# Kernel tuning notes

Measured on AMD Instinct MI355X. Metric: run time of the kernel, lower is better.

The kernel has to match this reference:

```python
import jax, jax.numpy as jnp
import numpy as np

HEADS, DIM_HEAD, LANDMARKS, PINV_ITERS = 8, 64, 256, 6


def moore_penrose_pinv(x, iters=PINV_ITERS):
    abs_x = jnp.abs(x)
    col = abs_x.sum(-1)
    row = abs_x.sum(-2)
    z = jnp.swapaxes(x, -1, -2) / (jnp.max(col) * jnp.max(row))
    I = jnp.eye(x.shape[-1], dtype=x.dtype)
    for _ in range(iters):
        xz = x @ z
        z = 0.25 * z @ (13 * I - xz @ (15 * I - xz @ (7 * I - xz)))
    return z


def nystrom_attention(x, w_qkv, w_out, b_out, res_conv_w):
    b, n, dim = x.shape
    m = LANDMARKS
    pad = (m - n % m) % m
    x = jnp.pad(x, ((0, 0), (pad, 0), (0, 0)))  # pad at front like F.pad(x,(0,0,pad,0))
    npad = n + pad
    qkv = x @ w_qkv  # (b, npad, 3*heads*dim_head)
    q, k, v = jnp.split(qkv, 3, axis=-1)
    sh = lambda t: t.reshape(b, npad, HEADS, DIM_HEAD).transpose(0, 2, 1, 3)
    q, k, v = sh(q), sh(k), sh(v)  # (b,h,npad,dh)
    q = q * (DIM_HEAD ** -0.5)
    l = npad // m
    q_l = q.reshape(b, HEADS, m, l, DIM_HEAD).mean(axis=3)  # landmarks (b,h,m,dh)
    k_l = k.reshape(b, HEADS, m, l, DIM_HEAD).mean(axis=3)
    attn1 = jax.nn.softmax(jnp.einsum('bhid,bhjd->bhij', q, k_l), -1)   # (b,h,npad,m)
    attn2 = jax.nn.softmax(jnp.einsum('bhid,bhjd->bhij', q_l, k_l), -1)  # (b,h,m,m)
    attn3 = jax.nn.softmax(jnp.einsum('bhid,bhjd->bhij', q_l, k), -1)   # (b,h,m,npad)
    out = attn1 @ (moore_penrose_pinv(attn2) @ (attn3 @ v))  # (b,h,npad,dh)
    # depthwise residual conv over sequence dim (Conv2d(heads,heads,(33,1),groups=heads,bias=False))
    res = jax.lax.conv_general_dilated(v, res_conv_w, (1, 1), ((16, 16), (0, 0)),
                                       dimension_numbers=('NCHW', 'OIHW', 'NCHW'),
                                       feature_group_count=HEADS)
    out = out + res
    out = out.transpose(0, 2, 1, 3).reshape(b, npad, HEADS * DIM_HEAD)
    out = out @ w_out + b_out
    return out[:, -n:]


def camil_forward(bag, adj_row, adj_col, adj_val, w_qkv, w_out, b_out, res_conv_w,
                  wq, wk, wv_w, wv_b, v_att, u_att, w_att, fc_kernel, fc_bias):
    N = bag.shape[1]
    # encoder
    xg = nystrom_attention(bag, w_qkv, w_out, b_out, res_conv_w)[0]  # (N,D)
    enc = xg + bag  # (1,N,D)
    q = enc @ wq  # (1,N,256)
    k = enc @ wk
    attn = jnp.einsum('bnd,bmd->bnm', q, k)[0] / jnp.sqrt(jnp.float32(256.0))  # (N,N)
    # sparse adjacency-masked neighbor aggregation
    edge_scores = adj_val * attn[adj_row, adj_col]
    A_raw = jax.ops.segment_sum(edge_scores, adj_row, num_segments=N)  # (N,)
    alpha = jax.nn.softmax(A_raw)
    value = bag @ wv_w + wv_b  # (1,N,D)
    xl = alpha[:, None] * value  # (1,N,D)
    wei2 = jax.nn.sigmoid(-xl) ** 2
    xo = xl * 2 * wei2 + 2 * enc * (1 - wei2)  # (1,N,D)
    # gated MIL attention (softmax over dim 0 of size 1, as in original)
    inst = jnp.tanh(xo @ v_att) * jax.nn.sigmoid(xo @ u_att)
    scores = inst @ w_att  # (1,N,1)
    k_alpha = jax.nn.softmax(scores, axis=0)
    attn_output = k_alpha * xo
    pooled = attn_output[0].sum(axis=0, keepdims=True)  # (1,D)
    out = pooled @ fc_kernel + fc_bias  # (1,1)
    return out, A_raw, k_alpha


def setup_inputs() -> dict:
    key = jax.random.key(0)
    ks = jax.random.split(key, 16)
    N, D, E = 10000, 512, 90000
    s = 0.02
    return {
        'bag': jax.random.normal(ks[0], (1, N, D), jnp.float32),
        'adj_row': jax.random.randint(ks[1], (E,), 0, N),
        'adj_col': jax.random.randint(ks[2], (E,), 0, N),
        'adj_val': jax.random.uniform(ks[3], (E,), jnp.float32),
        'w_qkv': jax.random.normal(ks[4], (D, 3 * HEADS * DIM_HEAD), jnp.float32) * s,
        'w_out': jax.random.normal(ks[5], (HEADS * DIM_HEAD, D), jnp.float32) * s,
        'b_out': jnp.zeros((D,), jnp.float32),
        'res_conv_w': jax.random.normal(ks[6], (HEADS, 1, 33, 1), jnp.float32) * s,
        'wq': jax.random.normal(ks[7], (D, 256), jnp.float32) * s,
        'wk': jax.random.normal(ks[8], (D, 256), jnp.float32) * s,
        'wv_w': jax.random.normal(ks[9], (D, D), jnp.float32) * s,
        'wv_b': jnp.zeros((D,), jnp.float32),
        'v_att': jax.random.normal(ks[10], (D, 128), jnp.float32) * s,
        'u_att': jax.random.normal(ks[11], (D, 128), jnp.float32) * s,
        'w_att': jax.random.normal(ks[12], (128, 1), jnp.float32) * s,
        'fc_kernel': jax.random.normal(ks[13], (D, 1), jnp.float32) * s,
        'fc_bias': jnp.zeros((1,), jnp.float32),
    }


def reference(bag, adj_row, adj_col, adj_val, w_qkv, w_out, b_out, res_conv_w,
              wq, wk, wv_w, wv_b, v_att, u_att, w_att, fc_kernel, fc_bias):
    return camil_forward(bag, adj_row, adj_col, adj_val, w_qkv, w_out, b_out, res_conv_w,
                         wq, wk, wv_w, wv_b, v_att, u_att, w_att, fc_kernel, fc_bias)
```

## Files before the change

### kernel.cpp

```cpp
#include <hip/hip_runtime.h>
#include <hip/hip_bf16.h>
#include <math.h>

#define NSEQ   10000
#define NPAD   10240
#define PADR   240
#define HEADS  8
#define DH     64
#define LM     256
#define LFAC   40
#define DMODEL 512
#define DQK    256
#define OUTSZ  20001
#define NSPLIT 16
#define KCH    128

typedef __attribute__((ext_vector_type(8))) short bf16x8;
typedef __attribute__((ext_vector_type(4))) float f32x4;
#define MFMA16(a,b,c) __builtin_amdgcn_mfma_f32_16x16x32_bf16(a,b,c,0,0,0)

typedef __attribute__((address_space(1))) const unsigned char gconst_t;
typedef __attribute__((address_space(3))) unsigned char lds_t;
#define GLD16(gp, lp) __builtin_amdgcn_global_load_lds((gconst_t*)(gp), (lds_t*)(lp), 16, 0, 0)

__device__ __forceinline__ float b2f(ushort u) {
    return __uint_as_float(((unsigned)u) << 16);
}
__device__ __forceinline__ ushort f2b(float f) {
    unsigned u = __float_as_uint(f);
    unsigned r = (u + 0x7FFFu + ((u >> 16) & 1u)) >> 16;
    return (ushort)r;
}
__device__ __forceinline__ int swz8(int bid, int nwg) {
    int q = nwg >> 3, r = nwg & 7;
    int x = bid & 7, idx = bid >> 3;
    int start = (x < r) ? x * (q + 1) : r * (q + 1) + (x - r) * q;
    return start + idx;
}
__device__ __forceinline__ f32x4 tr4(f32x4 v, int p) {
    f32x4 u, w;
    float s, r;
    s = (p & 1) ? v[0] : v[1]; r = __shfl_xor(s, 1);
    u[0] = (p & 1) ? r : v[0]; u[1] = (p & 1) ? v[1] : r;
    s = (p & 1) ? v[2] : v[3]; r = __shfl_xor(s, 1);
    u[2] = (p & 1) ? r : v[2]; u[3] = (p & 1) ? v[3] : r;
    s = (p & 2) ? u[0] : u[2]; r = __shfl_xor(s, 2);
    w[0] = (p & 2) ? r : u[0]; w[2] = (p & 2) ? u[2] : r;
    s = (p & 2) ? u[1] : u[3]; r = __shfl_xor(s, 2);
    w[1] = (p & 2) ? r : u[1]; w[3] = (p & 2) ? u[3] : r;
    return w;
}

__global__ __launch_bounds__(256)
void cvt_k(const float* __restrict__ in, ushort* __restrict__ out, int n4,
           float* __restrict__ outbuf, const float* __restrict__ fcb,
           unsigned int* __restrict__ mx)
{
    int i = blockIdx.x * 256 + threadIdx.x;
    if (i < n4) {
        float4 v = ((const float4*)in)[i];
        ushort4 u; u.x = f2b(v.x); u.y = f2b(v.y); u.z = f2b(v.z); u.w = f2b(v.w);
        ((ushort4*)out)[i] = u;
    }
    if (i == 0) { outbuf[0] = fcb[0]; mx[0] = 0u; mx[1] = 0u; }
    if (i >= 1 && i <= NSEQ) outbuf[i] = 0.f;
    if (i >= NSEQ + 1 && i < OUTSZ) outbuf[i] = 1.0f;
}

__global__ __launch_bounds__(256)
void wtrans_k(const float* __restrict__ w_qkv, const float* __restrict__ w_out,
              const float* __restrict__ wq, const float* __restrict__ wk,
              const float* __restrict__ wv_w,
              ushort* __restrict__ wqkvT, ushort* __restrict__ woutT,
              ushort* __restrict__ wqkT)
{
    __shared__ float tile[32][33];
    int g0 = blockIdx.x * 32, r0 = blockIdx.y * 32;
    const float* in; ushort* outp; int C; int lc0;
    if (g0 < 1536)      { in = w_qkv; outp = wqkvT;                      C = 1536; lc0 = g0; }
    else if (g0 < 2048) { in = w_out; outp = woutT;                      C = 512;  lc0 = g0 - 1536; }
    else if (g0 < 2304) { in = wq;    outp = wqkT;                       C = 256;  lc0 = g0 - 2048; }
    else if (g0 < 2560) { in = wk;    outp = wqkT + 256*512;             C = 256;  lc0 = g0 - 2304; }
    else                { in = wv_w;  outp = wqkvT + (size_t)1536*512;   C = 512;  lc0 = g0 - 2560; }
    int tx = threadIdx.x & 31, ty = threadIdx.x >> 5;
    for (int i = ty; i < 32; i += 8) tile[i][tx] = in[(size_t)(r0 + i) * C + lc0 + tx];
    __syncthreads();
    for (int i = ty; i < 32; i += 8) outp[(size_t)(lc0 + i) * 512 + r0 + tx] = f2b(tile[tx][i]);
}

template<int MODE, int TN>
__global__ __launch_bounds__(256)
void mgemm(const ushort* __restrict__ A, const ushort* __restrict__ Bt,
           int Mlog, int N, int K, int padr, int nbx,
           void* __restrict__ P0, void* __restrict__ P1, void* __restrict__ P2,
           void* __restrict__ P3, void* __restrict__ P4,
           const float* __restrict__ bias, const ushort* __restrict__ extra)
{
    constexpr int NF = TN / 32;
    constexpr int BSB = TN * 64;
    __shared__ __align__(16) char As[2 * 8192];
    __shared__ __align__(16) char Bs[2 * BSB];
    const int tid = threadIdx.x;
    const int l = tid & 63, w = tid >> 6;
    const int wm = w >> 1, wn = w & 1;
    const int wk_ = swz8(blockIdx.x, gridDim.x);
    const int row0 = (wk_ / nbx) * 128, col0 = (wk_ % nbx) * TN;
    const int lr = l & 15, lg = l >> 4;
    const bool slow = (MODE == 0) && (row0 < padr);
    const int NT = K >> 5;
    f32x4 acc[4][NF];
    #pragma unroll
    for (int i = 0; i < 4; ++i)
        #pragma unroll
        for (int j = 0; j < NF; ++j) acc[i][j] = (f32x4){0.f, 0.f, 0.f, 0.f};

    auto stage = [&](int bf, int t) {
        int k0 = t << 5;
        if (!slow) {
            #pragma unroll
            for (int c = 0; c < 2; ++c) {
                int q = w * 2 + c;
                int row = q * 16 + (l >> 2);
                GLD16(A + (size_t)(row0 + row - padr) * K + k0 + (l & 3) * 8,
                      As + bf * 8192 + q * 1024);
            }
            if (TN == 128) {
                #pragma unroll
                for (int c = 0; c < 2; ++c) {
                    int q = w * 2 + c;
                    int row = q * 16 + (l >> 2);
                    GLD16(Bt + (size_t)(col0 + row) * K + k0 + (l & 3) * 8,
                          Bs + bf * BSB + q * 1024);
                }
            } else {
                int row = w * 16 + (l >> 2);
                GLD16(Bt + (size_t)(col0 + row) * K + k0 + (l & 3) * 8,
                      Bs + bf * BSB + w * 1024);
            }
        } else {
            #pragma unroll
            for (int c = 0; c < 2; ++c) {
                int gidx = c * 256 + tid;
                int row = gidx >> 2, gr = gidx & 3;
                int phys = row0 + row - padr;
                uint4 v = {0, 0, 0, 0};
                if (phys >= 0 && phys < Mlog - padr)
                    v = *(const uint4*)(A + (size_t)phys * K + k0 + gr * 8);
                *(uint4*)(As + bf * 8192 + gidx * 16) = v;
            }
            if (TN == 128) {
                #pragma unroll
                for (int c = 0; c < 2; ++c) {
                    int gidx = c * 256 + tid;
                    int row = gidx >> 2, gr = gidx & 3;
                    *(uint4*)(Bs + bf * BSB + gidx * 16) =
                        *(const uint4*)(Bt + (size_t)(col0 + row) * K + k0 + gr * 8);
                }
            } else {
                int row = tid >> 2, gr = tid & 3;
                *(uint4*)(Bs + bf * BSB + tid * 16) =
                    *(const uint4*)(Bt + (size_t)(col0 + row) * K + k0 + gr * 8);
            }
        }
    };

    int cur = 0;
    stage(0, 0);
    __syncthreads();
    for (int t = 0; t < NT; ++t) {
        if (t + 1 < NT) stage(cur ^ 1, t + 1);
        const char* Ab = As + cur * 8192;
        const char* Bb = Bs + cur * BSB;
        bf16x8 af[4];
        #pragma unroll
        for (int mf = 0; mf < 4; ++mf)
            af[mf] = *(const bf16x8*)(Ab + (wm * 64 + mf * 16 + lr) * 64 + lg * 16);
        #pragma unroll
        for (int nf = 0; nf < NF; ++nf) {
            bf16x8 bfr = *(const bf16x8*)(Bb + (wn * (TN / 2) + nf * 16 + lr) * 64 + lg * 16);
            #pragma unroll
            for (int mf = 0; mf < 4; ++mf)
                acc[mf][nf] = MFMA16(af[mf], bfr, acc[mf][nf]);
        }
        __syncthreads();
        cur ^= 1;
    }

    const int p = lr & 3;
    #pragma unroll
    for (int mf = 0; mf < 4; ++mf)
    #pragma unroll
    for (int nf = 0; nf < NF; ++nf) {
        int cb   = col0 + wn * (TN / 2) + nf * 16 + (lr & 12);
        int rowT = row0 + wm * 64 + mf * 16 + lg * 4 + p;
        if (MODE == 0) {
            int c = col0 + wn * (TN / 2) + nf * 16 + lr;
            if ((c >> 9) == 2) {
                int hh = (c >> 6) & 7;
                int kt  = (row0 + wm * 64 + mf * 16 + lg * 4) >> 5;
                int lgp = ((mf * 2) + (lg >> 1)) & 3;
                int lanep = lr + lgp * 16;
                int e0 = (lg & 1) * 4;
                ushort4 pk;
                pk.x = f2b(acc[mf][nf][0]); pk.y = f2b(acc[mf][nf][1]);
                pk.z = f2b(acc[mf][nf][2]); pk.w = f2b(acc[mf][nf][3]);
                *(ushort4*)&((ushort*)P3)[(((size_t)hh * (NPAD/32) + kt) * 4 + (nf & 3)) * 512
                                          + lanep * 8 + e0] = pk;
            }
            int t = cb >> 9;
            f32x4 v = acc[mf][nf];
            if (t == 0) { v[0] *= 0.125f; v[1] *= 0.125f; v[2] *= 0.125f; v[3] *= 0.125f; }
            f32x4 wv = tr4(v, p);
            ushort4 pk;
            pk.x = f2b(wv[0]); pk.y = f2b(wv[1]); pk.z = f2b(wv[2]); pk.w = f2b(wv[3]);
            if (t < 3) {
                int hh = (cb >> 6) & 7, d0 = cb & 63;
                ushort* dst = (t == 0) ? (ushort*)P0 : (t == 1) ? (ushort*)P1 : (ushort*)P2;
                *(ushort4*)&dst[((size_t)hh * NPAD + rowT) * DH + d0] = pk;
            } else {
                int phys = rowT - PADR;
                if (phys >= 0)
                    *(ushort4*)&((ushort*)P4)[(size_t)phys * DMODEL + (cb & 511)] = pk;
            }
        } else if (MODE == 1) {
            f32x4 wv = tr4(acc[mf][nf], p);
            if (rowT < Mlog) {
                float4 bi = *(const float4*)(bias + cb);
                ushort4 bg = *(const ushort4*)(extra + (size_t)rowT * N + cb);
                float o0 = wv[0] + bi.x + b2f(bg.x), o1 = wv[1] + bi.y + b2f(bg.y);
                float o2 = wv[2] + bi.z + b2f(bg.z), o3 = wv[3] + bi.w + b2f(bg.w);
                ushort4 pk; pk.x = f2b(o0); pk.y = f2b(o1); pk.z = f2b(o2); pk.w = f2b(o3);
                *(ushort4*)&((ushort*)P1)[(size_t)rowT * N + cb] = pk;
            }
        } else if (MODE == 6) {
            f32x4 wv = tr4(acc[mf][nf], p);
            if (rowT < Mlog) {
                ushort4 pk;
                pk.x = f2b(wv[0]); pk.y = f2b(wv[1]); pk.z = f2b(wv[2]); pk.w = f2b(wv[3]);
                if (cb < 256)
                    *(ushort4*)&((ushort*)P0)[(size_t)rowT * 256 + cb] = pk;
                else
                    *(ushort4*)&((ushort*)P1)[(size_t)rowT * 256 + (cb - 256)] = pk;
            }
        }
    }
}

template<bool PLAIN, bool BCI, bool WPK>
__global__ __launch_bounds__(256)
void pinv_k(const ushort* __restrict__ A, const ushort* __restrict__ Bt,
            int N, float cval, float scale,
            ushort* __restrict__ P0, ushort* __restrict__ P1)
{
    __shared__ __align__(16) char smem[49152];
    char* As = smem;
    char* Bs = smem + 16384;
    const int tid = threadIdx.x, l = tid & 63, w = tid >> 6;
    const int lr = l & 15, lg = l >> 4;
    const int col0 = blockIdx.x * 64, row0 = blockIdx.y * 32, h = blockIdx.z;
    const ushort* Ab = A + (size_t)h * 65536;
    const ushort* Btb = Bt + (size_t)h * ((size_t)N * 256);
    {
        int row = tid >> 3, seg = (tid & 7) * 64;
        const uint4* sa = (const uint4*)(Ab + (size_t)(row0 + row) * 256) + (tid & 7) * 4;
        #pragma unroll
        for (int e = 0; e < 4; ++e) {
            int off = (row * 512 + seg + e * 16) ^ ((row & 7) << 4);
            *(uint4*)(As + off) = sa[e];
        }
    }
    {
        int row = tid >> 2, seg = (tid & 3) * 128;
        const uint4* sb = (const uint4*)(Btb + (size_t)(col0 + row) * 256) + (tid & 3) * 8;
        int gn = col0 + row;
        #pragma unroll
        for (int e = 0; e < 8; ++e) {
            int off = (row * 512 + seg + e * 16) ^ ((row & 7) << 4);
            uint4 vb = sb[e];
            if (BCI) {
                union { uint4 u; ushort s[8]; } t; t.u = vb;
                int gk0 = (seg >> 1) + e * 8;
                #pragma unroll
                for (int j = 0; j < 8; ++j)
                    t.s[j] = f2b(((gn == gk0 + j) ? cval : 0.f) - b2f(t.s[j]));
                vb = t.u;
            }
            *(uint4*)(Bs + off) = vb;
        }
    }
    __syncthreads();
    f32x4 acc[2];
    acc[0] = (f32x4){0.f, 0.f, 0.f, 0.f};
    acc[1] = (f32x4){0.f, 0.f, 0.f, 0.f};
    #pragma unroll
    for (int ks = 0; ks < 8; ++ks) {
        bf16x8 af[2];
        #pragma unroll
        for (int mf = 0; mf < 2; ++mf) {
            int ar = mf * 16 + lr;
            af[mf] = *(const bf16x8*)(As + ((ar * 512 + ks * 64 + lg * 16) ^ ((ar & 7) << 4)));
        }
        int br = w * 16 + lr;
        bf16x8 bf = *(const bf16x8*)(Bs + ((br * 512 + ks * 64 + lg * 16) ^ ((br & 7) << 4)));
        acc[0] = MFMA16(af[0], bf, acc[0]);
        acc[1] = MFMA16(af[1], bf, acc[1]);
    }
    #pragma unroll
    for (int mf = 0; mf < 2; ++mf) {
        int r0v = row0 + mf * 16 + lg * 4;
        int c = col0 + w * 16 + lr;
        if (PLAIN) {
            #pragma unroll
            for (int i = 0; i < 4; ++i)
                P0[(size_t)h * 256 * N + (size_t)(r0v + i) * N + c] = f2b(acc[mf][i] * scale);
        }
        ushort4 pk;
        pk.x = f2b(acc[mf][0] * scale); pk.y = f2b(acc[mf][1] * scale);
        pk.z = f2b(acc[mf][2] * scale); pk.w = f2b(acc[mf][3] * scale);
        if (WPK) {
            int off = (((c >> 4) * 8 + (r0v >> 5)) << 9) + (((r0v >> 3) & 3) << 7)
                    + ((c & 15) << 3) + (r0v & 4);
            *(ushort4*)&P1[(size_t)h * 16384 + off] = pk;
        } else {
            *(ushort4*)&P1[(size_t)h * ((size_t)N * 256) + (size_t)c * 256 + r0v] = pk;
        }
    }
}

__global__ __launch_bounds__(256)
void ns2_k(const ushort* __restrict__ P, const ushort* __restrict__ Pt,
           const ushort* __restrict__ Z,
           ushort* __restrict__ Qt, ushort* __restrict__ V1)
{
    __shared__ __align__(16) char smem[49152];
    char* As = smem;
    char* Bs = smem + 16384;
    const int tid = threadIdx.x, l = tid & 63, w = tid >> 6;
    const int lr = l & 15, lg = l >> 4;
    const int col0 = blockIdx.x * 64;
    const int which = blockIdx.y >> 3;
    const int row0 = (blockIdx.y & 7) * 32;
    const int h = blockIdx.z;
    const ushort* Ab = (which ? Z : P) + (size_t)h * 65536;
    const ushort* Btb = Pt + (size_t)h * 65536;
    {
        int row = tid >> 3, seg = (tid & 7) * 64;
        const uint4* sa = (const uint4*)(Ab + (size_t)(row0 + row) * 256) + (tid & 7) * 4;
        #pragma unroll
        for (int e = 0; e < 4; ++e) {
            int off = (row * 512 + seg + e * 16) ^ ((row & 7) << 4);
            *(uint4*)(As + off) = sa[e];
        }
    }
    {
        int row = tid >> 2, seg = (tid & 3) * 128;
        const uint4* sb = (const uint4*)(Btb + (size_t)(col0 + row) * 256) + (tid & 3) * 8;
        int gn = col0 + row;
        #pragma unroll
        for (int e = 0; e < 8; ++e) {
            int off = (row * 512 + seg + e * 16) ^ ((row & 7) << 4);
            uint4 vb = sb[e];
            if (which == 0) {
                union { uint4 u; ushort s[8]; } t; t.u = vb;
                int gk0 = (seg >> 1) + e * 8;
                #pragma unroll
                for (int j = 0; j < 8; ++j)
                    t.s[j] = f2b(((gn == gk0 + j) ? 7.f : 0.f) - b2f(t.s[j]));
                vb = t.u;
            }
            *(uint4*)(Bs + off) = vb;
        }
    }
    __syncthreads();
    f32x4 acc[2];
    acc[0] = (f32x4){0.f, 0.f, 0.f, 0.f};
    acc[1] = (f32x4){0.f, 0.f, 0.f, 0.f};
    #pragma unroll
    for (int ks = 0; ks < 8; ++ks) {
        bf16x8 af[2];
        #pragma unroll
        for (int mf = 0; mf < 2; ++mf) {
            int ar = mf * 16 + lr;
            af[mf] = *(const bf16x8*)(As + ((ar * 512 + ks * 64 + lg * 16) ^ ((ar & 7) << 4)));
        }
        int br = w * 16 + lr;
        bf16x8 bf = *(const bf16x8*)(Bs + ((br * 512 + ks * 64 + lg * 16) ^ ((br & 7) << 4)));
        acc[0] = MFMA16(af[0], bf, acc[0]);
        acc[1] = MFMA16(af[1], bf, acc[1]);
    }
    #pragma unroll
    for (int mf = 0; mf < 2; ++mf) {
        int r0v = row0 + mf * 16 + lg * 4;
        int c = col0 + w * 16 + lr;
        if (which == 0) {
            ushort4 pk;
            pk.x = f2b(acc[mf][0]); pk.y = f2b(acc[mf][1]);
            pk.z = f2b(acc[mf][2]); pk.w = f2b(acc[mf][3]);
            *(ushort4*)&Qt[(size_t)h * 65536 + (size_t)c * 256 + r0v] = pk;
        } else {
            #pragma unroll
            for (int i = 0; i < 4; ++i)
                V1[(size_t)h * 65536 + (size_t)(r0v + i) * 256 + c] = f2b(acc[mf][i]);
        }
    }
}

__global__ __launch_bounds__(256)
void ns3_k(const ushort* __restrict__ V1, const ushort* __restrict__ Qt,
           const ushort* __restrict__ Z,
           ushort* __restrict__ Zn, ushort* __restrict__ Znt)
{
    __shared__ __align__(16) char smem[49152];
    char* As = smem;
    char* Bs = smem + 16384;
    const int tid = threadIdx.x, l = tid & 63, w = tid >> 6;
    const int lr = l & 15, lg = l >> 4;
    const int col0 = blockIdx.x * 64, row0 = blockIdx.y * 32, h = blockIdx.z;
    const ushort* Ab = V1 + (size_t)h * 65536;
    const ushort* Btb = Qt + (size_t)h * 65536;
    {
        int row = tid >> 3, seg = (tid & 7) * 64;
        const uint4* sa = (const uint4*)(Ab + (size_t)(row0 + row) * 256) + (tid & 7) * 4;
        #pragma unroll
        for (int e = 0; e < 4; ++e) {
            int off = (row * 512 + seg + e * 16) ^ ((row & 7) << 4);
            *(uint4*)(As + off) = sa[e];
        }
    }
    {
        int row = tid >> 2, seg = (tid & 3) * 128;
        const uint4* sb = (const uint4*)(Btb + (size_t)(col0 + row) * 256) + (tid & 3) * 8;
        #pragma unroll
        for (int e = 0; e < 8; ++e) {
            int off = (row * 512 + seg + e * 16) ^ ((row & 7) << 4);
            *(uint4*)(Bs + off) = sb[e];
        }
    }
    __syncthreads();
    f32x4 acc[2];
    acc[0] = (f32x4){0.f, 0.f, 0.f, 0.f};
    acc[1] = (f32x4){0.f, 0.f, 0.f, 0.f};
    #pragma unroll
    for (int ks = 0; ks < 8; ++ks) {
        bf16x8 af[2];
        #pragma unroll
        for (int mf = 0; mf < 2; ++mf) {
            int ar = mf * 16 + lr;
            af[mf] = *(const bf16x8*)(As + ((ar * 512 + ks * 64 + lg * 16) ^ ((ar & 7) << 4)));
        }
        int br = w * 16 + lr;
        bf16x8 bf = *(const bf16x8*)(Bs + ((br * 512 + ks * 64 + lg * 16) ^ ((br & 7) << 4)));
        acc[0] = MFMA16(af[0], bf, acc[0]);
        acc[1] = MFMA16(af[1], bf, acc[1]);
    }
    #pragma unroll
    for (int mf = 0; mf < 2; ++mf) {
        int r0v = row0 + mf * 16 + lg * 4;
        int c = col0 + w * 16 + lr;
        ushort4 pk;
        #pragma unroll
        for (int i = 0; i < 4; ++i) {
            size_t idx = (size_t)h * 65536 + (size_t)(r0v + i) * 256 + c;
            float o = 0.25f * acc[mf][i] + 3.25f * b2f(Z[idx]) - 3.75f * b2f(V1[idx]);
            ushort u = f2b(o);
            Zn[idx] = u;
            ((ushort*)&pk)[i] = u;
        }
        *(ushort4*)&Znt[(size_t)h * 65536 + (size_t)c * 256 + r0v] = pk;
    }
}

__global__ void landmark2_k(const ushort* __restrict__ Qb, const ushort* __restrict__ Kb,
                            ushort* __restrict__ QLb, ushort* __restrict__ KLb,
                            ushort* __restrict__ KLpk)
{
    int b = blockIdx.x;
    bool isK = b >= HEADS * LM;
    if (isK) b -= HEADS * LM;
    int hh = b >> 8, j = b & 255, d = threadIdx.x;
    const ushort* p = (isK ? Kb : Qb) + ((size_t)hh * NPAD + (size_t)j * LFAC) * DH + d;
    float s = 0.f;
    #pragma unroll
    for (int t = 0; t < LFAC; ++t) s += b2f(p[t * DH]);
    ushort u = f2b(s * (1.f / LFAC));
    (isK ? KLb : QLb)[((size_t)hh * LM + j) * DH + d] = u;
    if (isK) {
        int nf = j >> 4, lr = j & 15;
        int ks = d >> 5, lg = (d >> 3) & 3, e = d & 7;
        KLpk[(((size_t)hh * 16 + nf) * 2 + ks) * 512 + (lg * 16 + lr) * 8 + e] = u;
    }
}

__global__ __launch_bounds__(256)
void attn2_k(const ushort* __restrict__ QL, const ushort* __restrict__ KL,
             ushort* __restrict__ X2b)
{
    int i = blockIdx.x, h = blockIdx.y, j = threadIdx.x;
    __shared__ float qv[DH];
    __shared__ float red[256];
    if (j < DH) qv[j] = b2f(QL[((size_t)h * LM + i) * DH + j]);
    __syncthreads();
    const uint4* kp = (const uint4*)(KL + ((size_t)h * LM + j) * DH);
    float dot = 0.f;
    #pragma unroll
    for (int cc = 0; cc < 8; ++cc) {
        union { uint4 u; ushort s[8]; } uu; uu.u = kp[cc];
        #pragma unroll
        for (int e = 0; e < 8; ++e) dot += qv[cc * 8 + e] * b2f(uu.s[e]);
    }
    red[j] = dot; __syncthreads();
    for (int s = 128; s > 0; s >>= 1) { if (j < s) red[j] = fmaxf(red[j], red[j + s]); __syncthreads(); }
    float mx = red[0]; __syncthreads();
    float e = __expf(dot - mx);
    red[j] = e; __syncthreads();
    for (int s = 128; s > 0; s >>= 1) { if (j < s) red[j] += red[j + s]; __syncthreads(); }
    X2b[((size_t)h * LM + i) * LM + j] = f2b(e / red[0]);
}

__global__ __launch_bounds__(256)
void colrow_k(const ushort* __restrict__ X2b, unsigned int* __restrict__ mx)
{
    int h = blockIdx.x, t = threadIdx.x;
    const ushort* x = X2b + (size_t)h * LM * LM;
    float rs = 0.f;
    for (int i = 0; i < LM; ++i) rs += fabsf(b2f(x[(size_t)i * LM + t]));
    __shared__ float r2[256];
    r2[t] = rs; __syncthreads();
    for (int s = 128; s > 0; s >>= 1) {
        if (t < s) r2[t] = fmaxf(r2[t], r2[t + s]);
        __syncthreads();
    }
    if (t == 0) atomicMax(&mx[1], __float_as_uint(r2[0]));
}

__global__ void zinit_k(const ushort* __restrict__ X2b, const float* __restrict__ mxf,
                        ushort* __restrict__ Z, ushort* __restrict__ Zt)
{
    int i = blockIdx.x, h = blockIdx.y, j = threadIdx.x;
    float scale = 1.f / mxf[1];
    float x = b2f(X2b[((size_t)h * LM + i) * LM + j]) * scale;
    ushort u = f2b(x);
    Z[((size_t)h * LM + j) * LM + i] = u;
    Zt[((size_t)h * LM + i) * LM + j] = u;
}

__global__ __launch_bounds__(256)
void attn3_fa(const ushort* __restrict__ QLb, const ushort* __restrict__ Kb,
              const ushort* __restrict__ VtPk,
              float* __restrict__ Opart, float* __restrict__ Mpart,
              float* __restrict__ Lpart)
{
    __shared__ __align__(16) char smem[9216 + 18432];
    ushort* Qs = (ushort*)smem;
    ushort* Ks = (ushort*)(smem + 9216);
    ushort* Ps = (ushort*)(smem + 9216);
    const int tid = threadIdx.x, l = tid & 63, wv = tid >> 6;
    const int split = blockIdx.x, qt = blockIdx.y, h = blockIdx.z;
    const int lr = l & 15, lg = l >> 4;
    {
        int row = tid >> 2, seg = (tid & 3) * 16;
        const uint4* src = (const uint4*)(QLb + ((size_t)h * LM + qt * 64 + row) * DH + seg);
        *(uint4*)&Qs[row * 72 + seg] = src[0];
        *(uint4*)&Qs[row * 72 + seg + 8] = src[1];
    }
    f32x4 o[4];
    float m_[4], l_[4];
    #pragma unroll
    for (int nf = 0; nf < 4; ++nf) o[nf] = (f32x4){0.f, 0.f, 0.f, 0.f};
    #pragma unroll
    for (int i = 0; i < 4; ++i) { m_[i] = -INFINITY; l_[i] = 0.f; }
    const int k0base = split * (NPAD / NSPLIT);
    for (int ch = 0; ch < NPAD / NSPLIT / KCH; ++ch) {
        int kg0 = k0base + ch * KCH;
        __syncthreads();
        {
            int row = tid >> 1, half = (tid & 1) * 32;
            const uint4* src = (const uint4*)(Kb + ((size_t)h * NPAD + kg0 + row) * DH + half);
            #pragma unroll
            for (int e = 0; e < 4; ++e) *(uint4*)&Ks[row * 72 + half + e * 8] = src[e];
        }
        __syncthreads();
        f32x4 s[8];
        #pragma unroll
        for (int nf = 0; nf < 8; ++nf) s[nf] = (f32x4){0.f, 0.f, 0.f, 0.f};
        #pragma unroll
        for (int ks = 0; ks < 2; ++ks) {
            bf16x8 a = *(const bf16x8*)&Qs[(wv * 16 + lr) * 72 + ks * 32 + lg * 8];
            #pragma unroll
            for (int nf = 0; nf < 8; ++nf) {
                bf16x8 b = *(const bf16x8*)&Ks[(nf * 16 + lr) * 72 + ks * 32 + lg * 8];
                s[nf] = MFMA16(a, b, s[nf]);
            }
        }
        float scl[4];
        #pragma unroll
        for (int i = 0; i < 4; ++i) {
            float mx = s[0][i];
            #pragma unroll
            for (int nf = 1; nf < 8; ++nf) mx = fmaxf(mx, s[nf][i]);
            mx = fmaxf(mx, __shfl_xor(mx, 1)); mx = fmaxf(mx, __shfl_xor(mx, 2));
            mx = fmaxf(mx, __shfl_xor(mx, 4)); mx = fmaxf(mx, __shfl_xor(mx, 8));
            float mn = fmaxf(m_[i], mx);
            float sum = 0.f;
            #pragma unroll
            for (int nf = 0; nf < 8; ++nf) {
                float e = __expf(s[nf][i] - mn); s[nf][i] = e; sum += e;
            }
            sum += __shfl_xor(sum, 1); sum += __shfl_xor(sum, 2);
            sum += __shfl_xor(sum, 4); sum += __shfl_xor(sum, 8);
            float sc = __expf(m_[i] - mn);
            l_[i] = l_[i] * sc + sum;
            m_[i] = mn;
            scl[i] = sc;
        }
        #pragma unroll
        for (int nf = 0; nf < 4; ++nf)
        #pragma unroll
        for (int i = 0; i < 4; ++i) o[nf][i] *= scl[i];
        __syncthreads();
        #pragma unroll
        for (int nf = 0; nf < 8; ++nf)
        #pragma unroll
        for (int i = 0; i < 4; ++i) {
            int row = wv * 16 + lg * 4 + i;
            int col = nf * 16 + lr;
            Ps[row * 128 + (col ^ ((row & 7) << 3))] = f2b(s[nf][i]);
        }
        #pragma unroll
        for (int ks = 0; ks < 4; ++ks) {
            int row = wv * 16 + lr;
            int kcol = ks * 32 + lg * 8;
            bf16x8 a = *(const bf16x8*)&Ps[row * 128 + (kcol ^ ((row & 7) << 3))];
            int kgt = (kg0 >> 5) + ks;
            #pragma unroll
            for (int nf = 0; nf < 4; ++nf) {
                bf16x8 b = *(const bf16x8*)(VtPk +
                    (((size_t)h * (NPAD/32) + kgt) * 4 + nf) * 512 + (size_t)l * 8);
                o[nf] = MFMA16(a, b, o[nf]);
            }
        }
    }
    const int base = (split * 4 + qt) * 8 + h;
    #pragma unroll
    for (int nf = 0; nf < 4; ++nf)
    #pragma unroll
    for (int i = 0; i < 4; ++i) {
        int r = wv * 16 + lg * 4 + i;
        int c = nf * 16 + lr;
        Opart[((size_t)base * 64 + r) * 64 + c] = o[nf][i];
    }
    if (lr == 0) {
        #pragma unroll
        for (int i = 0; i < 4; ++i) {
            int r = wv * 16 + lg * 4 + i;
            Mpart[base * 64 + r] = m_[i];
            Lpart[base * 64 + r] = l_[i];
        }
    }
}

__global__ __launch_bounds__(256)
void mergeAV_k(const float* __restrict__ Opart, const float* __restrict__ Mpart,
               const float* __restrict__ Lpart, ushort* __restrict__ AVt)
{
    int qt = blockIdx.x, h = blockIdx.y, rq = blockIdx.z;
    int t = threadIdx.x;
    int r = rq * 32 + (t >> 3), c0 = (t & 7) * 8;
    float mv[NSPLIT];
    float mstar = -INFINITY;
    #pragma unroll
    for (int s = 0; s < NSPLIT; ++s) {
        mv[s] = Mpart[((s * 4 + qt) * 8 + h) * 64 + r];
        mstar = fmaxf(mstar, mv[s]);
    }
    float wgt[NSPLIT];
    float L = 0.f;
    #pragma unroll
    for (int s = 0; s < NSPLIT; ++s) {
        wgt[s] = __expf(mv[s] - mstar);
        L += wgt[s] * Lpart[((s * 4 + qt) * 8 + h) * 64 + r];
    }
    float inv = 1.f / L;
    float acc[8] = {};
    #pragma unroll
    for (int s = 0; s < NSPLIT; ++s) {
        const float* op = Opart + (((size_t)(s * 4 + qt) * 8 + h) * 64 + r) * 64 + c0;
        #pragma unroll
        for (int e = 0; e < 8; ++e) acc[e] += wgt[s] * op[e];
    }
    #pragma unroll
    for (int e = 0; e < 8; ++e)
        AVt[((size_t)h * DH + c0 + e) * LM + qt * 64 + r] = f2b(acc[e] * inv);
}

__global__ __launch_bounds__(256)
void conv_k(const ushort* __restrict__ Vb, const float* __restrict__ cw,
            ushort* __restrict__ OBc)
{
    int idx = blockIdx.x * 256 + threadIdx.x;
    if (idx >= NSEQ * 128) return;
    int ro = idx >> 7, c4 = idx & 127;
    int h = c4 >> 4, dq = (c4 & 15) * 4;
    int i = ro + PADR;
    float a0 = 0, a1 = 0, a2 = 0, a3 = 0;
    #pragma unroll
    for (int tt = 0; tt < 33; ++tt) {
        int src = i + tt - 16;
        if (src < NPAD) {
            float wv = cw[h * 33 + tt];
            ushort4 u = *(const ushort4*)(Vb + ((size_t)h * NPAD + src) * DH + dq);
            a0 += wv * b2f(u.x); a1 += wv * b2f(u.y);
            a2 += wv * b2f(u.z); a3 += wv * b2f(u.w);
        }
    }
    ushort4 o; o.x = f2b(a0); o.y = f2b(a1); o.z = f2b(a2); o.w = f2b(a3);
    *(ushort4*)&OBc[(size_t)ro * DMODEL + h * DH + dq] = o;
}

__global__ __launch_bounds__(256, 4)
void outrows64v2(const ushort* __restrict__ Qb, const ushort* __restrict__ KLpk,
                 const ushort* __restrict__ Wpk, const ushort* __restrict__ OBc,
                 ushort* __restrict__ OBb)
{
    __shared__ __align__(16) char smem[40960];
    char*   Qs  = smem;
    ushort* KLs = (ushort*)(smem + 8192);
    ushort* Ps  = (ushort*)(smem + 8192);
    const int tid = threadIdx.x, l = tid & 63, w = tid >> 6;
    const int h = blockIdx.y, i0 = blockIdx.x * 64;
    const int lr = l & 15, lg = l >> 4;

    ushort obc[4][4];
    #pragma unroll
    for (int nf = 0; nf < 4; ++nf)
    #pragma unroll
    for (int i = 0; i < 4; ++i) {
        int r = i0 + w * 16 + lg * 4 + i;
        obc[nf][i] = (r >= PADR)
            ? OBc[(size_t)(r - PADR) * DMODEL + h * DH + nf * 16 + lr] : (ushort)0;
    }
    {
        int row = tid >> 2;
        int seg = (tid & 3) * 32;
        const uint4* src = (const uint4*)(Qb + ((size_t)h * NPAD + i0 + row) * DH) + (tid & 3) * 2;
        uint4 v0 = src[0], v1 = src[1];
        int sw = (row & 7) << 4;
        *(uint4*)(Qs + row * 128 + (seg ^ sw)) = v0;
        *(uint4*)(Qs + row * 128 + ((seg + 16) ^ sw)) = v1;
    }
    {
        const uint4* src = (const uint4*)(KLpk + (size_t)h * 16384) + tid;
        uint4* dst = (uint4*)KLs + tid;
        #pragma unroll
        for (int e = 0; e < 8; ++e) dst[e * 256] = src[e * 256];
    }
    __syncthreads();

    f32x4 s[16];
    #pragma unroll
    for (int nf = 0; nf < 16; ++nf) s[nf] = (f32x4){0.f, 0.f, 0.f, 0.f};
    #pragma unroll
    for (int ks = 0; ks < 2; ++ks) {
        int qrow = w * 16 + lr;
        bf16x8 a = *(const bf16x8*)(Qs + qrow * 128 +
                                    ((ks * 64 + lg * 16) ^ ((qrow & 7) << 4)));
        #pragma unroll
        for (int nf = 0; nf < 16; ++nf) {
            bf16x8 b = *(const bf16x8*)&KLs[((nf * 2 + ks) * 64 + l) * 8];
            s[nf] = MFMA16(a, b, s[nf]);
        }
    }
    float inv_[4];
    #pragma unroll
    for (int i = 0; i < 4; ++i) {
        float m = s[0][i];
        #pragma unroll
        for (int nf = 1; nf < 16; ++nf) m = fmaxf(m, s[nf][i]);
        m = fmaxf(m, __shfl_xor(m, 1)); m = fmaxf(m, __shfl_xor(m, 2));
        m = fmaxf(m, __shfl_xor(m, 4)); m = fmaxf(m, __shfl_xor(m, 8));
        float sum = 0.f;
        #pragma unroll
        for (int nf = 0; nf < 16; ++nf) {
            float e = __expf(s[nf][i] - m); s[nf][i] = e; sum += e;
        }
        sum += __shfl_xor(sum, 1); sum += __shfl_xor(sum, 2);
        sum += __shfl_xor(sum, 4); sum += __shfl_xor(sum, 8);
        inv_[i] = 1.f / sum;
    }
    __syncthreads();
    #pragma unroll
    for (int nf = 0; nf < 16; ++nf)
    #pragma unroll
    for (int i = 0; i < 4; ++i) {
        int row = w * 16 + lg * 4 + i;
        int col = nf * 16 + lr;
        Ps[row * 256 + (col ^ ((row & 7) << 3))] = f2b(s[nf][i] * inv_[i]);
    }
    f32x4 o[4];
    #pragma unroll
    for (int nf = 0; nf < 4; ++nf) o[nf] = (f32x4){0.f, 0.f, 0.f, 0.f};
    #pragma unroll
    for (int ks = 0; ks < 8; ++ks) {
        int row = w * 16 + lr;
        int kcol = ks * 32 + lg * 8;
        bf16x8 a = *(const bf16x8*)&Ps[row * 256 + (kcol ^ ((row & 7) << 3))];
        #pragma unroll
        for (int nf = 0; nf < 4; ++nf) {
            bf16x8 b = *(const bf16x8*)(Wpk + (((size_t)h * 2048) + nf * 512 + ks * 64 + l) * 8);
            o[nf] = MFMA16(a, b, o[nf]);
        }
    }
    #pragma unroll
    for (int nf = 0; nf < 4; ++nf)
    #pragma unroll
    for (int i = 0; i < 4; ++i) {
        int r = i0 + w * 16 + lg * 4 + i;
        if (r >= PADR) {
            int ro = r - PADR;
            int c = h * DH + nf * 16 + lr;
            OBb[(size_t)ro * DMODEL + c] = f2b(o[nf][i] + b2f(obc[nf][i]));
        }
    }
}

__global__ __launch_bounds__(256)
void edges_k(const int* __restrict__ rows, const int* __restrict__ cols,
             const float* __restrict__ vals,
             const ushort* __restrict__ QE, const ushort* __restrict__ KE,
             float* __restrict__ A_raw, int E)
{
    int gid = blockIdx.x * blockDim.x + threadIdx.x;
    int e = gid >> 4, l = gid & 15;
    if (e >= E) return;
    int r = rows[e], c = cols[e];
    const uint4* qp = (const uint4*)(QE + (size_t)r * DQK + l * 16);
    const uint4* kp = (const uint4*)(KE + (size_t)c * DQK + l * 16);
    float dot = 0.f;
    #pragma unroll
    for (int g = 0; g < 2; ++g) {
        union { uint4 u; ushort s[8]; } qq, kk;
        qq.u = qp[g]; kk.u = kp[g];
        #pragma unroll
        for (int j = 0; j < 8; ++j) dot += b2f(qq.s[j]) * b2f(kk.s[j]);
    }
    dot += __shfl_xor(dot, 8); dot += __shfl_xor(dot, 4);
    dot += __shfl_xor(dot, 2); dot += __shfl_xor(dot, 1);
    if (l == 0) atomicAdd(&A_raw[r], vals[e] * dot * 0.0625f);
}

__global__ __launch_bounds__(1024)
void alphasm_k(const float* __restrict__ A_raw, float* __restrict__ alpha)
{
    __shared__ float red[1024];
    int t = threadIdx.x;
    float lm = -INFINITY;
    for (int i = t; i < NSEQ; i += 1024) lm = fmaxf(lm, A_raw[i]);
    red[t] = lm; __syncthreads();
    for (int s = 512; s > 0; s >>= 1) { if (t < s) red[t] = fmaxf(red[t], red[t + s]); __syncthreads(); }
    float mx = red[0]; __syncthreads();
    float ls = 0.f;
    for (int i = t; i < NSEQ; i += 1024) ls += __expf(A_raw[i] - mx);
    red[t] = ls; __syncthreads();
    for (int s = 512; s > 0; s >>= 1) { if (t < s) red[t] += red[t + s]; __syncthreads(); }
    float inv = 1.f / red[0];
    for (int i = t; i < NSEQ; i += 1024) alpha[i] = __expf(A_raw[i] - mx) * inv;
}

__global__ __launch_bounds__(256)
void xo_pooled_k(const ushort* __restrict__ VALb, const ushort* __restrict__ ENCb,
                 const float* __restrict__ alpha, const float* __restrict__ wvb,
                 const float* __restrict__ fck, float* __restrict__ out0)
{
    __shared__ float red[256];
    int t = threadIdx.x;
    float acc = 0.f;
    const int total = NSEQ * 128;
    for (int idx = blockIdx.x * 256 + t; idx < total; idx += gridDim.x * 256) {
        int r = idx >> 7, dq = (idx & 127) * 4;
        float al = alpha[r];
        ushort4 v4 = *(const ushort4*)(VALb + (size_t)r * DMODEL + dq);
        ushort4 e4 = *(const ushort4*)(ENCb + (size_t)r * DMODEL + dq);
        float4 b4 = *(const float4*)(wvb + dq);
        float4 f4 = *(const float4*)(fck + dq);
        float vv[4] = {b2f(v4.x) + b4.x, b2f(v4.y) + b4.y,
                       b2f(v4.z) + b4.z, b2f(v4.w) + b4.w};
        float ee[4] = {b2f(e4.x), b2f(e4.y), b2f(e4.z), b2f(e4.w)};
        float ff[4] = {f4.x, f4.y, f4.z, f4.w};
        #pragma unroll
        for (int j = 0; j < 4; ++j) {
            float xl = al * vv[j];
            float s = 1.f / (1.f + __expf(xl));
            float w2 = s * s;
            float xo = 2.f * xl * w2 + 2.f * ee[j] * (1.f - w2);
            acc += xo * ff[j];
        }
    }
    red[t] = acc; __syncthreads();
    for (int s = 128; s > 0; s >>= 1) { if (t < s) red[t] += red[t + s]; __syncthreads(); }
    if (t == 0) atomicAdd(out0, red[0]);
}

extern "C" void kernel_launch(void* const* d_in, const int* in_sizes, int n_in,
                              void* d_out, int out_size, void* d_ws, size_t ws_size,
                              hipStream_t stream)
{
    (void)n_in; (void)out_size; (void)ws_size;
    const float* bag   = (const float*)d_in[0];
    const int*   arow  = (const int*)d_in[1];
    const int*   acol  = (const int*)d_in[2];
    const float* aval  = (const float*)d_in[3];
    const float* w_qkv = (const float*)d_in[4];
    const float* w_out = (const float*)d_in[5];
    const float* b_out = (const float*)d_in[6];
    const float* convw = (const float*)d_in[7];
    const float* wq    = (const float*)d_in[8];
    const float* wk    = (const float*)d_in[9];
    const float* wv_w  = (const float*)d_in[10];
    const float* wv_b  = (const float*)d_in[11];
    const float* fck   = (const float*)d_in[15];
    const float* fcb   = (const float*)d_in[16];
    const int E = in_sizes[1];
    float* out = (float*)d_out;

    char* ws = (char*)d_ws;
    size_t off = 0;
    auto alloc = [&](size_t bytes) { void* p = ws + off; off += (bytes + 255) & ~(size_t)255; return p; };
    ushort* Qb    = (ushort*)alloc((size_t)HEADS * NPAD * DH * 2);
    ushort* Kb    = (ushort*)alloc((size_t)HEADS * NPAD * DH * 2);
    ushort* Vb    = (ushort*)alloc((size_t)HEADS * NPAD * DH * 2);
    ushort* bagb  = (ushort*)alloc((size_t)NSEQ * DMODEL * 2);
    ushort* wqkvT = (ushort*)alloc((size_t)2048 * 512 * 2);
    ushort* woutT = (ushort*)alloc((size_t)512 * 512 * 2);
    ushort* wqkT  = (ushort*)alloc((size_t)512 * 512 * 2);
    ushort* VALb  = (ushort*)alloc((size_t)NSEQ * DMODEL * 2);
    ushort* QLb   = (ushort*)alloc((size_t)HEADS * LM * DH * 2);
    ushort* KLb   = (ushort*)alloc((size_t)HEADS * LM * DH * 2);
    ushort* KLpk  = (ushort*)alloc((size_t)HEADS * LM * DH * 2);
    ushort* Wpk   = (ushort*)alloc((size_t)HEADS * DH * LM * 2);
    ushort* X2b   = (ushort*)alloc((size_t)HEADS * LM * LM * 2);
    ushort* Za    = (ushort*)alloc((size_t)HEADS * LM * LM * 2);
    ushort* Zat   = (ushort*)alloc((size_t)HEADS * LM * LM * 2);
    ushort* Zb2   = (ushort*)alloc((size_t)HEADS * LM * LM * 2);
    ushort* Zbt2  = (ushort*)alloc((size_t)HEADS * LM * LM * 2);
    ushort* T0    = (ushort*)alloc((size_t)HEADS * LM * LM * 2);
    ushort* T0t   = (ushort*)alloc((size_t)HEADS * LM * LM * 2);
    ushort* T1t   = (ushort*)alloc((size_t)HEADS * LM * LM * 2);
    ushort* T2t   = (ushort*)alloc((size_t)HEADS * LM * LM * 2);
    ushort* AVt   = (ushort*)alloc((size_t)HEADS * DH * LM * 2);
    ushort* OBc   = (ushort*)alloc((size_t)NSEQ * DMODEL * 2);
    ushort* OBb   = (ushort*)alloc((size_t)NSEQ * DMODEL * 2);
    float*  ENCf  = (float*)alloc((size_t)NSEQ * DMODEL * 4);
    ushort* ENCb  = (ushort*)alloc((size_t)NSEQ * DMODEL * 2);
    float*  ALPHA = (float*)alloc((size_t)NPAD * 4);
    float*  MXf   = (float*)alloc(256);
    unsigned int* MX = (unsigned int*)MXf;
    ushort* QEb = Qb;
    ushort* KEb = Kb;
    ushort* VtPk  = (ushort*)ENCf;
    float*  Opart = (float*)ENCb;
    float*  Mpart = (float*)((char*)ENCb + 8388608);
    float*  Lpart = (float*)((char*)ENCb + 8519680);

    cvt_k<<<(NSEQ * DMODEL / 4 + 255) / 256, 256, 0, stream>>>(
        bag, bagb, NSEQ * DMODEL / 4, out, fcb, MX);
    wtrans_k<<<dim3(96, 16), 256, 0, stream>>>(w_qkv, w_out, wq, wk, wv_w,
                                               wqkvT, woutT, wqkT);

    mgemm<0, 128><<<1280, 256, 0, stream>>>(
        bagb, wqkvT, NPAD, 2048, 512, PADR, 16,
        Qb, Kb, Vb, VtPk, VALb, nullptr, nullptr);

    landmark2_k<<<2 * HEADS * LM, DH, 0, stream>>>(Qb, Kb, QLb, KLb, KLpk);

    attn2_k<<<dim3(LM, HEADS), 256, 0, stream>>>(QLb, KLb, X2b);
    colrow_k<<<HEADS, 256, 0, stream>>>(X2b, MX);
    zinit_k<<<dim3(LM, HEADS), 256, 0, stream>>>(X2b, MXf, Za, Zat);

    ushort *Z = Za, *Zt = Zat, *Zn = Zb2, *Znt = Zbt2;
    for (int it = 0; it < 6; ++it) {
        pinv_k<true, false, false><<<dim3(4, 8, HEADS), 256, 0, stream>>>(
            X2b, Zt, LM, 0.f, 1.f, T0, T0t);
        ns2_k<<<dim3(4, 16, HEADS), 256, 0, stream>>>(T0, T0t, Z, T1t, T2t);
        ns3_k<<<dim3(4, 8, HEADS), 256, 0, stream>>>(T2t, T1t, Z, Zn, Znt);
        ushort* t;
        t = Z; Z = Zn; Zn = t;
        t = Zt; Zt = Znt; Znt = t;
    }

    attn3_fa<<<dim3(NSPLIT, 4, HEADS), 256, 0, stream>>>(QLb, Kb, VtPk, Opart, Mpart, Lpart);
    mergeAV_k<<<dim3(4, HEADS, 2), 256, 0, stream>>>(Opart, Mpart, Lpart, AVt);
    pinv_k<false, false, true><<<dim3(1, 8, HEADS), 256, 0, stream>>>(
        Za, AVt, DH, 0.f, 1.f, nullptr, Wpk);

    conv_k<<<(NSEQ * 128 + 255) / 256, 256, 0, stream>>>(Vb, convw, OBc);
    outrows64v2<<<dim3(NPAD / 64, HEADS), 256, 0, stream>>>(Qb, KLpk, Wpk, OBc, OBb);

    mgemm<1, 64><<<632, 256, 0, stream>>>(
        OBb, woutT, NSEQ, DMODEL, 512, 0, 8,
        nullptr, ENCb, nullptr, nullptr, nullptr, b_out, bagb);

    mgemm<6, 64><<<632, 256, 0, stream>>>(
        ENCb, wqkT, NSEQ, 512, 512, 0, 8,
        QEb, KEb, nullptr, nullptr, nullptr, nullptr, nullptr);

    edges_k<<<(E * 16 + 255) / 256, 256, 0, stream>>>(arow, acol, aval, QEb, KEb, out + 1, E);
    alphasm_k<<<1, 1024, 0, stream>>>(out + 1, ALPHA);

    xo_pooled_k<<<1280, 256, 0, stream>>>(VALb, ENCb, ALPHA, wv_b, fck, out);
}
```

Baseline: 345.0 us.

## Fuse landmark and conv kernels; parallelize alpha softmax across blocks

Merges the landmark-mean kernel into the depthwise conv kernel as one launch with two block roles, which removes a launch and lets the small landmark work overlap with the conv. The single-block 1024-thread softmax over alpha is replaced by a multi-block max (atomicMax on an order-preserving uint encoding), a multi-block exp-and-sum (atomicAdd), and normalization folded into xo_pooled. This adds one launch and float atomics, so the summation order becomes nondeterministic.

```diff
diff --git a/kernel.cpp b/kernel.cpp
--- a/kernel.cpp
+++ b/kernel.cpp
@@ -31,6 +31,13 @@
     unsigned r = (u + 0x7FFFu + ((u >> 16) & 1u)) >> 16;
     return (ushort)r;
 }
+__device__ __forceinline__ unsigned fenc(float f) {
+    unsigned u = __float_as_uint(f);
+    return (u & 0x80000000u) ? ~u : (u | 0x80000000u);
+}
+__device__ __forceinline__ float fdec(unsigned k) {
+    return __uint_as_float((k & 0x80000000u) ? (k & 0x7FFFFFFFu) : ~k);
+}
 __device__ __forceinline__ int swz8(int bid, int nwg) {
     int q = nwg >> 3, r = nwg & 7;
     int x = bid & 7, idx = bid >> 3;
@@ -62,7 +69,12 @@
         ushort4 u; u.x = f2b(v.x); u.y = f2b(v.y); u.z = f2b(v.z); u.w = f2b(v.w);
         ((ushort4*)out)[i] = u;
     }
-    if (i == 0) { outbuf[0] = fcb[0]; mx[0] = 0u; mx[1] = 0u; }
+    if (i == 0) {
+        outbuf[0] = fcb[0];
+        mx[0] = 0u; mx[1] = 0u;
+        mx[2] = 0u;
+        ((float*)mx)[3] = 0.f;
+    }
     if (i >= 1 && i <= NSEQ) outbuf[i] = 0.f;
     if (i >= NSEQ + 1 && i < OUTSZ) outbuf[i] = 1.0f;
 }
@@ -470,24 +482,49 @@
     }
 }
 
-__global__ void landmark2_k(const ushort* __restrict__ Qb, const ushort* __restrict__ Kb,
-                            ushort* __restrict__ QLb, ushort* __restrict__ KLb,
-                            ushort* __restrict__ KLpk)
-{
-    int b = blockIdx.x;
-    bool isK = b >= HEADS * LM;
-    if (isK) b -= HEADS * LM;
-    int hh = b >> 8, j = b & 255, d = threadIdx.x;
-    const ushort* p = (isK ? Kb : Qb) + ((size_t)hh * NPAD + (size_t)j * LFAC) * DH + d;
-    float s = 0.f;
-    #pragma unroll
-    for (int t = 0; t < LFAC; ++t) s += b2f(p[t * DH]);
-    ushort u = f2b(s * (1.f / LFAC));
-    (isK ? KLb : QLb)[((size_t)hh * LM + j) * DH + d] = u;
-    if (isK) {
-        int nf = j >> 4, lr = j & 15;
-        int ks = d >> 5, lg = (d >> 3) & 3, e = d & 7;
-        KLpk[(((size_t)hh * 16 + nf) * 2 + ks) * 512 + (lg * 16 + lr) * 8 + e] = u;
+__global__ __launch_bounds__(256)
+void landconv_k(const ushort* __restrict__ Qb, const ushort* __restrict__ Kb,
+                const ushort* __restrict__ Vb, const float* __restrict__ cw,
+                ushort* __restrict__ OBc,
+                ushort* __restrict__ QLb, ushort* __restrict__ KLb,
+                ushort* __restrict__ KLpk)
+{
+    int bid = blockIdx.x;
+    if (bid < 5000) {
+        int idx = bid * 256 + threadIdx.x;
+        int ro = idx >> 7, c4 = idx & 127;
+        int h = c4 >> 4, dq = (c4 & 15) * 4;
+        int i = ro + PADR;
+        float a0 = 0, a1 = 0, a2 = 0, a3 = 0;
+        #pragma unroll
+        for (int tt = 0; tt < 33; ++tt) {
+            int src = i + tt - 16;
+            if (src < NPAD) {
+                float wv = cw[h * 33 + tt];
+                ushort4 u = *(const ushort4*)(Vb + ((size_t)h * NPAD + src) * DH + dq);
+                a0 += wv * b2f(u.x); a1 += wv * b2f(u.y);
+                a2 += wv * b2f(u.z); a3 += wv * b2f(u.w);
+            }
+        }
+        ushort4 o; o.x = f2b(a0); o.y = f2b(a1); o.z = f2b(a2); o.w = f2b(a3);
+        *(ushort4*)&OBc[(size_t)ro * DMODEL + h * DH + dq] = o;
+    } else {
+        int gidx = (bid - 5000) * 4 + (threadIdx.x >> 6);
+        int d = threadIdx.x & 63;
+        bool isK = gidx >= HEADS * LM;
+        int b = isK ? gidx - HEADS * LM : gidx;
+        int hh = b >> 8, j = b & 255;
+        const ushort* p = (isK ? Kb : Qb) + ((size_t)hh * NPAD + (size_t)j * LFAC) * DH + d;
+        float s = 0.f;
+        #pragma unroll
+        for (int t = 0; t < LFAC; ++t) s += b2f(p[t * DH]);
+        ushort u = f2b(s * (1.f / LFAC));
+        (isK ? KLb : QLb)[((size_t)hh * LM + j) * DH + d] = u;
+        if (isK) {
+            int nf = j >> 4, lr = j & 15;
+            int ks = d >> 5, lg = (d >> 3) & 3, e = d & 7;
+            KLpk[(((size_t)hh * 16 + nf) * 2 + ks) * 512 + (lg * 16 + lr) * 8 + e] = u;
+        }
     }
 }
 
@@ -693,30 +730,6 @@
         AVt[((size_t)h * DH + c0 + e) * LM + qt * 64 + r] = f2b(acc[e] * inv);
 }
 
-__global__ __launch_bounds__(256)
-void conv_k(const ushort* __restrict__ Vb, const float* __restrict__ cw,
-            ushort* __restrict__ OBc)
-{
-    int idx = blockIdx.x * 256 + threadIdx.x;
-    if (idx >= NSEQ * 128) return;
-    int ro = idx >> 7, c4 = idx & 127;
-    int h = c4 >> 4, dq = (c4 & 15) * 4;
-    int i = ro + PADR;
-    float a0 = 0, a1 = 0, a2 = 0, a3 = 0;
-    #pragma unroll
-    for (int tt = 0; tt < 33; ++tt) {
-        int src = i + tt - 16;
-        if (src < NPAD) {
-            float wv = cw[h * 33 + tt];
-            ushort4 u = *(const ushort4*)(Vb + ((size_t)h * NPAD + src) * DH + dq);
-            a0 += wv * b2f(u.x); a1 += wv * b2f(u.y);
-            a2 += wv * b2f(u.z); a3 += wv * b2f(u.w);
-        }
-    }
-    ushort4 o; o.x = f2b(a0); o.y = f2b(a1); o.z = f2b(a2); o.w = f2b(a3);
-    *(ushort4*)&OBc[(size_t)ro * DMODEL + h * DH + dq] = o;
-}
-
 __global__ __launch_bounds__(256, 4)
 void outrows64v2(const ushort* __restrict__ Qb, const ushort* __restrict__ KLpk,
                  const ushort* __restrict__ Wpk, const ushort* __restrict__ OBc,
@@ -848,36 +861,51 @@
     if (l == 0) atomicAdd(&A_raw[r], vals[e] * dot * 0.0625f);
 }
 
-__global__ __launch_bounds__(1024)
-void alphasm_k(const float* __restrict__ A_raw, float* __restrict__ alpha)
-{
-    __shared__ float red[1024];
+__global__ __launch_bounds__(256)
+void amax_k(const float* __restrict__ A_raw, unsigned int* __restrict__ mx)
+{
+    __shared__ float red[256];
     int t = threadIdx.x;
     float lm = -INFINITY;
-    for (int i = t; i < NSEQ; i += 1024) lm = fmaxf(lm, A_raw[i]);
+    for (int i = blockIdx.x * 256 + t; i < NSEQ; i += gridDim.x * 256)
+        lm = fmaxf(lm, A_raw[i]);
     red[t] = lm; __syncthreads();
-    for (int s = 512; s > 0; s >>= 1) { if (t < s) red[t] = fmaxf(red[t], red[t + s]); __syncthreads(); }
-    float mx = red[0]; __syncthreads();
-    float ls = 0.f;
-    for (int i = t; i < NSEQ; i += 1024) ls += __expf(A_raw[i] - mx);
-    red[t] = ls; __syncthreads();
-    for (int s = 512; s > 0; s >>= 1) { if (t < s) red[t] += red[t + s]; __syncthreads(); }
-    float inv = 1.f / red[0];
-    for (int i = t; i < NSEQ; i += 1024) alpha[i] = __expf(A_raw[i] - mx) * inv;
-}
-
-__global__ __launch_bounds__(256)
-void xo_pooled_k(const ushort* __restrict__ VALb, const ushort* __restrict__ ENCb,
-                 const float* __restrict__ alpha, const float* __restrict__ wvb,
-                 const float* __restrict__ fck, float* __restrict__ out0)
+    for (int s = 128; s > 0; s >>= 1) { if (t < s) red[t] = fmaxf(red[t], red[t + s]); __syncthreads(); }
+    if (t == 0) atomicMax(&mx[2], fenc(red[0]));
+}
+
+__global__ __launch_bounds__(256)
+void aexp_k(const float* __restrict__ A_raw, const unsigned int* __restrict__ mx,
+            float* __restrict__ alpha, float* __restrict__ sum)
 {
     __shared__ float red[256];
     int t = threadIdx.x;
+    float m = fdec(mx[2]);
+    float ls = 0.f;
+    for (int i = blockIdx.x * 256 + t; i < NSEQ; i += gridDim.x * 256) {
+        float e = __expf(A_raw[i] - m);
+        alpha[i] = e;
+        ls += e;
+    }
+    red[t] = ls; __syncthreads();
+    for (int s = 128; s > 0; s >>= 1) { if (t < s) red[t] += red[t + s]; __syncthreads(); }
+    if (t == 0) atomicAdd(sum, red[0]);
+}
+
+__global__ __launch_bounds__(256)
+void xo_pooled_k(const ushort* __restrict__ VALb, const ushort* __restrict__ ENCb,
+                 const float* __restrict__ alpha, const float* __restrict__ asum,
+                 const float* __restrict__ wvb, const float* __restrict__ fck,
+                 float* __restrict__ out0)
+{
+    __shared__ float red[256];
+    int t = threadIdx.x;
+    float inv_sum = 1.f / asum[0];
     float acc = 0.f;
     const int total = NSEQ * 128;
     for (int idx = blockIdx.x * 256 + t; idx < total; idx += gridDim.x * 256) {
         int r = idx >> 7, dq = (idx & 127) * 4;
-        float al = alpha[r];
+        float al = alpha[r] * inv_sum;
         ushort4 v4 = *(const ushort4*)(VALb + (size_t)r * DMODEL + dq);
         ushort4 e4 = *(const ushort4*)(ENCb + (size_t)r * DMODEL + dq);
         float4 b4 = *(const float4*)(wvb + dq);
@@ -970,7 +998,7 @@
         bagb, wqkvT, NPAD, 2048, 512, PADR, 16,
         Qb, Kb, Vb, VtPk, VALb, nullptr, nullptr);
 
-    landmark2_k<<<2 * HEADS * LM, DH, 0, stream>>>(Qb, Kb, QLb, KLb, KLpk);
+    landconv_k<<<6024, 256, 0, stream>>>(Qb, Kb, Vb, convw, OBc, QLb, KLb, KLpk);
 
     attn2_k<<<dim3(LM, HEADS), 256, 0, stream>>>(QLb, KLb, X2b);
     colrow_k<<<HEADS, 256, 0, stream>>>(X2b, MX);
@@ -992,7 +1020,6 @@
     pinv_k<false, false, true><<<dim3(1, 8, HEADS), 256, 0, stream>>>(
         Za, AVt, DH, 0.f, 1.f, nullptr, Wpk);
 
-    conv_k<<<(NSEQ * 128 + 255) / 256, 256, 0, stream>>>(Vb, convw, OBc);
     outrows64v2<<<dim3(NPAD / 64, HEADS), 256, 0, stream>>>(Qb, KLpk, Wpk, OBc, OBb);
 
     mgemm<1, 64><<<632, 256, 0, stream>>>(
@@ -1004,7 +1031,8 @@
         QEb, KEb, nullptr, nullptr, nullptr, nullptr, nullptr);
 
     edges_k<<<(E * 16 + 255) / 256, 256, 0, stream>>>(arow, acol, aval, QEb, KEb, out + 1, E);
-    alphasm_k<<<1, 1024, 0, stream>>>(out + 1, ALPHA);
-
-    xo_pooled_k<<<1280, 256, 0, stream>>>(VALb, ENCb, ALPHA, wv_b, fck, out);
-}
+    amax_k<<<40, 256, 0, stream>>>(out + 1, MX);
+    aexp_k<<<40, 256, 0, stream>>>(out + 1, MX, ALPHA, MXf + 3);
+
+    xo_pooled_k<<<1280, 256, 0, stream>>>(VALb, ENCb, ALPHA, MXf + 3, wv_b, fck, out);
+}
```

Result: no change. 343.7 us (-0.3%).
